# Performance work log

Hardware: AMD Instinct MI355X
Metric: run time of the kernel (lower is better)

Reference implementation:

```python
import jax, jax.numpy as jnp
import numpy as np


def setup_inputs() -> dict:
    key = jax.random.key(0)
    ks = jax.random.split(key, 6)
    B, C, W, H = 8, 512, 64, 64
    return {
        "x": jax.random.normal(ks[0], (B, C, W, H), dtype=jnp.float32),
        "proj_query": jax.random.normal(ks[1], (C, W, H), dtype=jnp.float32),
        "key_w": jax.random.normal(ks[2], (C, C), dtype=jnp.float32) * 0.02,
        "key_b": jax.random.normal(ks[3], (C,), dtype=jnp.float32) * 0.02,
        "value_w": jax.random.normal(ks[4], (C, C), dtype=jnp.float32) * 0.02,
        "value_b": jax.random.normal(ks[5], (C,), dtype=jnp.float32) * 0.02,
        "gamma": jnp.ones((1,), dtype=jnp.float32),
    }


def reference(x, proj_query, key_w, key_b, value_w, value_b, gamma):
    B, C, W, H = x.shape
    N = W * H
    # fixed memory query: (C, N); torch builds B x N x C via permute
    q = proj_query.reshape(C, N)
    # 1x1 convs == per-pixel channel matmuls
    k = jnp.einsum('oc,bchw->bohw', key_w, x) + key_b[None, :, None, None]
    v = jnp.einsum('oc,bchw->bohw', value_w, x) + value_b[None, :, None, None]
    k = k.reshape(B, C, N)
    v = v.reshape(B, C, N)
    # energy = bmm(key [B,C,N], query^T [N,C]) -> B x C x C (channel attention)
    energy = jnp.einsum('bcn,dn->bcd', k, q)
    attention = jax.nn.softmax(energy, axis=-1)
    # out = bmm(attention^T [B,C,C], value [B,C,N]) -> B x C x N
    out = jnp.einsum('bdc,bdn->bcn', attention, v)
    out = out.reshape(B, C, W, H)
    return gamma * out + x
```

## Files before the change

### kernel.cpp

```cpp
#include <hip/hip_runtime.h>

typedef unsigned short u16;
typedef unsigned int u32;
typedef unsigned long long u64;
typedef _Float16 f16x8 __attribute__((ext_vector_type(8)));
typedef float f32x4 __attribute__((ext_vector_type(4)));

__device__ __forceinline__ u16 f2h(float f) {
  union { _Float16 h; u16 u; } c; c.h = (_Float16)f; return c.u;
}
__device__ __forceinline__ float h2f(u16 v) {
  union { u16 u; _Float16 h; } c; c.u = v; return (float)c.h;
}

__device__ __forceinline__ f32x4 mfma16(f16x8 a, f16x8 b, f32x4 c) {
  return __builtin_amdgcn_mfma_f32_16x16x32_f16(a, b, c, 0, 0, 0);
}

__device__ __forceinline__ void ld8f(const float* s, u16* o) {
  float4 a = *(const float4*)s;
  float4 b = *(const float4*)(s + 4);
  o[0] = f2h(a.x); o[1] = f2h(a.y); o[2] = f2h(a.z); o[3] = f2h(a.w);
  o[4] = f2h(b.x); o[5] = f2h(b.y); o[6] = f2h(b.z); o[7] = f2h(b.w);
}

__device__ __forceinline__ void glds16(const u16* g, u16* l) {
  __builtin_amdgcn_global_load_lds(
      reinterpret_cast<const __attribute__((address_space(1))) u32*>(reinterpret_cast<u64>(g)),
      reinterpret_cast<__attribute__((address_space(3))) u32*>(reinterpret_cast<u64>(l)),
      16, 0, 0);
}

template<int TM, int TN, int WM, int WN, int DEPTH>
__device__ __forceinline__ void gemm_core(const u16* __restrict__ A, int lda,
                                          const u16* __restrict__ B, int ldb,
                                          int ksteps, u16* sA, u16* sB, f32x4 acc[TM][TN]) {
  constexpr int NT = WM * WN * 64;
  constexpr int BM = WM * TM * 16, BN = WN * TN * 16;
  constexpr int TILEA = BM * 32, TILEB = BN * 32;
  constexpr int APF = (BM * 4) / NT, BPF = (BN * 4) / NT;
  constexpr int VPI = APF + BPF;
  constexpr int PF = DEPTH - 2;
  static_assert(PF == 1 || PF == 2, "");
  static_assert(APF >= 1 && BPF >= 1, "");

  const int t = threadIdx.x;
  const int lane = t & 63, wave = t >> 6;
  const int wm = wave / WN, wn = wave % WN;
  const int m16 = lane & 15, q4 = lane >> 4;

  int aoff[APF], asl[APF];
#pragma unroll
  for (int p = 0; p < APF; ++p) {
    int s = p * NT + t, row = s >> 2;
    int kc = (s & 3) ^ ((row >> 1) & 3);
    aoff[p] = row * lda + kc * 8;
    asl[p] = (p * NT + (wave << 6)) * 8;
  }
  int boff[BPF], bsl[BPF];
#pragma unroll
  for (int p = 0; p < BPF; ++p) {
    int s = p * NT + t, row = s >> 2;
    int kc = (s & 3) ^ ((row >> 1) & 3);
    boff[p] = row * ldb + kc * 8;
    bsl[p] = (p * NT + (wave << 6)) * 8;
  }

  int aro[TM], bro[TN];
#pragma unroll
  for (int i = 0; i < TM; ++i) {
    int row = wm * TM * 16 + i * 16 + m16;
    aro[i] = row * 32 + ((q4 ^ ((row >> 1) & 3)) << 3);
  }
#pragma unroll
  for (int j = 0; j < TN; ++j) {
    int row = wn * TN * 16 + j * 16 + m16;
    bro[j] = row * 32 + ((q4 ^ ((row >> 1) & 3)) << 3);
  }

#pragma unroll
  for (int j = 0; j < PF; ++j) {
    const u16* Aj = A + j * 32;
    u16* aS = sA + j * TILEA;
#pragma unroll
    for (int p = 0; p < APF; ++p) glds16(Aj + aoff[p], aS + asl[p]);
    const u16* Bj = B + j * 32;
    u16* bS = sB + j * TILEB;
#pragma unroll
    for (int p = 0; p < BPF; ++p) glds16(Bj + boff[p], bS + bsl[p]);
  }

  int cur = 0, stg = PF;
#pragma unroll 1
  for (int kt = 0; kt < ksteps; ++kt) {
    if (kt + PF < ksteps) {
      const u16* An = A + (size_t)(kt + PF) * 32;
      u16* aS = sA + stg * TILEA;
#pragma unroll
      for (int p = 0; p < APF; ++p) glds16(An + aoff[p], aS + asl[p]);
      const u16* Bn = B + (size_t)(kt + PF) * 32;
      u16* bS = sB + stg * TILEB;
#pragma unroll
      for (int p = 0; p < BPF; ++p) glds16(Bn + boff[p], bS + bsl[p]);
    }
    if (PF == 2 && kt + 2 < ksteps)
      asm volatile("s_waitcnt vmcnt(%0)" :: "n"(2 * VPI) : "memory");
    else if (kt + 1 < ksteps)
      asm volatile("s_waitcnt vmcnt(%0)" :: "n"(VPI) : "memory");
    else
      asm volatile("s_waitcnt vmcnt(0)" ::: "memory");
    __builtin_amdgcn_s_barrier();
    __builtin_amdgcn_sched_barrier(0);

    const u16* aR = sA + cur * TILEA;
    const u16* bR = sB + cur * TILEB;
    f16x8 af[TM], bv[TN];
#pragma unroll
    for (int i = 0; i < TM; ++i) af[i] = *(const f16x8*)&aR[aro[i]];
#pragma unroll
    for (int j = 0; j < TN; ++j) bv[j] = *(const f16x8*)&bR[bro[j]];
#pragma unroll
    for (int i = 0; i < TM; ++i)
#pragma unroll
      for (int j = 0; j < TN; ++j)
        acc[i][j] = mfma16(af[i], bv[j], acc[i][j]);

    cur = (cur + 1 == DEPTH) ? 0 : cur + 1;
    stg = (stg + 1 == DEPTH) ? 0 : stg + 1;
  }
}

__global__ __launch_bounds__(256) void prep_all_kernel(const float* __restrict__ x,
                                                       u16* __restrict__ xh, u16* __restrict__ xhT,
                                                       const float* __restrict__ q, u16* __restrict__ qh,
                                                       float* __restrict__ qs,
                                                       const float* __restrict__ vw, u16* __restrict__ vwT,
                                                       const float* __restrict__ kw, u16* __restrict__ kwh,
                                                       float* __restrict__ beta) {
  __shared__ __align__(16) u16 T[64 * 72];
  int blk = blockIdx.x, t = threadIdx.x;
  if (blk < 4096) {
    int nt = blk & 63, ot = (blk >> 6) & 7, b = blk >> 9;
    int s = t & 31;
    int c = (t >> 5) * 8;

    const float* xp = x + ((size_t)b * 512 + ot * 64 + 2 * s) * 4096 + nt * 64 + c;
    u16 r0[8], r1[8];
    ld8f(xp, r0);
    ld8f(xp + 4096, r1);

    u16* xq = xh + ((size_t)b * 512 + ot * 64 + 2 * s) * 4096 + nt * 64 + c;
    *(int4*)xq = *(int4*)r0;
    *(int4*)(xq + 4096) = *(int4*)r1;

    u32* Tw = (u32*)T;
#pragma unroll
    for (int e = 0; e < 8; ++e)
      Tw[(c + e) * 36 + s] = (u32)r0[e] | ((u32)r1[e] << 16);
    __syncthreads();

    int rr = t >> 2, og = t & 3;
    int4 v0 = *(const int4*)&T[rr * 72 + og * 16];
    int4 v1 = *(const int4*)&T[rr * 72 + og * 16 + 8];
    u16* xo = xhT + ((size_t)b * 4096 + nt * 64 + rr) * 512 + ot * 64 + og * 16;
    *(int4*)xo = v0;
    *(int4*)(xo + 8) = v1;
  } else if (blk < 4608) {
    int row = blk - 4096;
    float s = 0.f;
#pragma unroll
    for (int p = 0; p < 2; ++p) {
      size_t i = (size_t)row * 4096 + p * 2048 + t * 8;
      u16 o[8];
      ld8f(q + i, o);
#pragma unroll
      for (int e = 0; e < 8; ++e) s += h2f(o[e]);
      *(int4*)&qh[i] = *(int4*)o;
    }
    for (int off = 32; off; off >>= 1) s += __shfl_xor(s, off);
    __shared__ float wsum[4];
    if ((t & 63) == 0) wsum[t >> 6] = s;
    __syncthreads();
    if (t == 0) qs[row] = wsum[0] + wsum[1] + wsum[2] + wsum[3];
  } else if (blk < 4864) {
    int bi = blk - 4608;
    u16* sT = T;
    int bx = bi & 15, by = bi >> 4;
#pragma unroll
    for (int p = 0; p < 4; ++p) {
      int idx = p * 256 + t; int r = idx >> 5, c = idx & 31;
      sT[r * 33 + c] = f2h(vw[(size_t)(by * 32 + r) * 512 + bx * 32 + c]);
    }
    __syncthreads();
#pragma unroll
    for (int p = 0; p < 4; ++p) {
      int idx = p * 256 + t; int r = idx >> 5, c = idx & 31;
      vwT[(size_t)(bx * 32 + r) * 512 + by * 32 + c] = sT[c * 33 + r];
    }
  } else if (blk < 4992) {
    size_t i = ((size_t)(blk - 4864) * 256 + t) * 8;
    u16 o[8];
    ld8f(kw + i, o);
    *(int4*)&kwh[i] = *(int4*)o;
  } else {
    for (int i = t; i < 4096; i += 256) beta[i] = 0.f;
  }
}

__global__ __launch_bounds__(256) void sgemm_kernel(const u16* __restrict__ qh, const u16* __restrict__ xh,
                                                    u16* __restrict__ Sh) {
  __shared__ __align__(16) u16 sA[4 * 64 * 32], sB[4 * 64 * 32];
  int rt = blockIdx.x, jt = blockIdx.y;
  f32x4 acc[2][2];
#pragma unroll
  for (int i = 0; i < 2; ++i)
#pragma unroll
    for (int j = 0; j < 2; ++j) acc[i][j] = (f32x4){0.f, 0.f, 0.f, 0.f};
  gemm_core<2, 2, 2, 2, 4>(qh + (size_t)jt * 64 * 4096, 4096,
                           xh + (size_t)rt * 64 * 4096, 4096, 128, sA, sB, acc);

  const int t = threadIdx.x, lane = t & 63, wave = t >> 6;
  const int wm = wave >> 1, wn = wave & 1, m16 = lane & 15, q4 = lane >> 4;
  int b = (rt * 64) >> 9, o0 = (rt * 64) & 511;
  u16* Ob = Sh + (size_t)b * 262144;
#pragma unroll
  for (int i = 0; i < 2; ++i)
#pragma unroll
    for (int j = 0; j < 2; ++j)
#pragma unroll
      for (int r = 0; r < 4; ++r) {
        int y = jt * 64 + wm * 32 + i * 16 + q4 * 4 + r;
        int o = o0 + wn * 32 + j * 16 + m16;
        Ob[(size_t)y * 512 + o] = f2h(acc[i][j][r]);
      }
}

__global__ __launch_bounds__(256) void egemm_kernel(const u16* __restrict__ kwh, const u16* __restrict__ Sh,
                                                    float* __restrict__ E) {
  __shared__ __align__(16) u16 sA[4 * 64 * 32], sB[4 * 64 * 32];
  int xt = blockIdx.x >> 3, yt = blockIdx.x & 7, b = blockIdx.y;
  f32x4 acc[2][2];
#pragma unroll
  for (int i = 0; i < 2; ++i)
#pragma unroll
    for (int j = 0; j < 2; ++j) acc[i][j] = (f32x4){0.f, 0.f, 0.f, 0.f};
  gemm_core<2, 2, 2, 2, 4>(kwh + (size_t)xt * 64 * 512, 512,
                           Sh + (size_t)b * 262144 + (size_t)yt * 64 * 512, 512, 16, sA, sB, acc);

  const int t = threadIdx.x, lane = t & 63, wave = t >> 6;
  const int wm = wave >> 1, wn = wave & 1, m16 = lane & 15, q4 = lane >> 4;
  float* O = E + ((size_t)b * 512 + xt * 64) * 512 + yt * 64;
#pragma unroll
  for (int i = 0; i < 2; ++i)
#pragma unroll
    for (int j = 0; j < 2; ++j)
#pragma unroll
      for (int r = 0; r < 4; ++r) {
        int row = wm * 32 + i * 16 + q4 * 4 + r;
        int col = wn * 32 + j * 16 + m16;
        O[(size_t)row * 512 + col] = acc[i][j][r];
      }
}

__global__ __launch_bounds__(256) void softmax_kernel(const float* __restrict__ E, const float* __restrict__ qs,
                                                      const float* __restrict__ kb, const float* __restrict__ vb,
                                                      u16* __restrict__ attT, float* __restrict__ beta) {
  __shared__ float sE[16 * 516];
  __shared__ float sM[16], sS[16];
  int i0 = blockIdx.x * 16, b = blockIdx.y, t = threadIdx.x;
  const float* Eb = E + ((size_t)b * 512 + i0) * 512;
  for (int ch = 0; ch < 32; ++ch) {
    int idx = ch * 256 + t;
    int row = idx >> 9, col = idx & 511;
    sE[row * 516 + col] = Eb[(size_t)row * 512 + col] + kb[i0 + row] * qs[col];
  }
  __syncthreads();
  {
    int row = t >> 4, sub = t & 15;
    float mx = -1e30f;
    for (int ii = 0; ii < 32; ++ii) mx = fmaxf(mx, sE[row * 516 + sub + ii * 16]);
    for (int off = 8; off; off >>= 1) mx = fmaxf(mx, __shfl_xor(mx, off));
    float sm = 0.f;
    for (int ii = 0; ii < 32; ++ii) sm += __expf(sE[row * 516 + sub + ii * 16] - mx);
    for (int off = 8; off; off >>= 1) sm += __shfl_xor(sm, off);
    if (sub == 0) { sM[row] = mx; sS[row] = 1.f / sm; }
  }
  __syncthreads();
  float vbr = vb[i0 + (t & 15)];
  u16* Ob = attT + (size_t)b * 262144;
  for (int ch = 0; ch < 32; ++ch) {
    int idx = ch * 256 + t;
    int r = idx & 15, j = idx >> 4;
    float a = __expf(sE[r * 516 + j] - sM[r]) * sS[r];
    Ob[(size_t)j * 512 + i0 + r] = f2h(a);
    float part = a * vbr;
    for (int off = 8; off; off >>= 1) part += __shfl_xor(part, off);
    if (r == 0) atomicAdd(&beta[b * 512 + j], part);
  }
}

__global__ __launch_bounds__(256) void wgemm_kernel(const u16* __restrict__ attT, const u16* __restrict__ vwT,
                                                    u16* __restrict__ W) {
  __shared__ __align__(16) u16 sA[4 * 64 * 32], sB[4 * 64 * 32];
  int ct = blockIdx.x >> 3, ot = blockIdx.x & 7, b = blockIdx.y;
  f32x4 acc[2][2];
#pragma unroll
  for (int i = 0; i < 2; ++i)
#pragma unroll
    for (int j = 0; j < 2; ++j) acc[i][j] = (f32x4){0.f, 0.f, 0.f, 0.f};
  gemm_core<2, 2, 2, 2, 4>(attT + (size_t)b * 262144 + (size_t)ct * 64 * 512, 512,
                           vwT + (size_t)ot * 64 * 512, 512, 16, sA, sB, acc);

  const int t = threadIdx.x, lane = t & 63, wave = t >> 6;
  const int wm = wave >> 1, wn = wave & 1, m16 = lane & 15, q4 = lane >> 4;
  u16* O = W + (size_t)b * 262144 + (size_t)(ct * 64) * 512 + ot * 64;
#pragma unroll
  for (int i = 0; i < 2; ++i)
#pragma unroll
    for (int j = 0; j < 2; ++j)
#pragma unroll
      for (int r = 0; r < 4; ++r) {
        int row = wm * 32 + i * 16 + q4 * 4 + r;
        int col = wn * 32 + j * 16 + m16;
        O[(size_t)row * 512 + col] = f2h(acc[i][j][r]);
      }
}

__global__ __launch_bounds__(512, 4) void outgemm_kernel(const u16* __restrict__ W, const u16* __restrict__ xhT,
                                                         const float* __restrict__ x, const float* __restrict__ beta,
                                                         const float* __restrict__ gm, float* __restrict__ out) {
  __shared__ __align__(16) u16 sA[3 * 128 * 32], sB[3 * 256 * 32];
  int nt = blockIdx.x, ct = blockIdx.y, b = blockIdx.z;
  f32x4 acc[4][4];
#pragma unroll
  for (int i = 0; i < 4; ++i)
#pragma unroll
    for (int j = 0; j < 4; ++j) acc[i][j] = (f32x4){0.f, 0.f, 0.f, 0.f};
  gemm_core<4, 4, 2, 4, 3>(W + (size_t)b * 262144 + (size_t)ct * 128 * 512, 512,
                           xhT + (size_t)b * 2097152 + (size_t)nt * 256 * 512, 512, 16, sA, sB, acc);

  const int t = threadIdx.x, lane = t & 63, wave = t >> 6;
  const int wm = wave >> 2, wn = wave & 3, m16 = lane & 15, q4 = lane >> 4;
  float g = gm[0];
#pragma unroll
  for (int i = 0; i < 4; ++i)
#pragma unroll
    for (int j = 0; j < 4; ++j)
#pragma unroll
      for (int r = 0; r < 4; ++r) {
        int c = ct * 128 + wm * 64 + i * 16 + q4 * 4 + r;
        int n = nt * 256 + wn * 64 + j * 16 + m16;
        size_t idx = (size_t)b * 2097152 + (size_t)c * 4096 + n;
        out[idx] = g * (acc[i][j][r] + beta[b * 512 + c]) + x[idx];
      }
}

extern "C" void kernel_launch(void* const* d_in, const int* in_sizes, int n_in,
                              void* d_out, int out_size, void* d_ws, size_t ws_size,
                              hipStream_t stream) {
  const float* x  = (const float*)d_in[0];
  const float* pq = (const float*)d_in[1];
  const float* kw = (const float*)d_in[2];
  const float* kb = (const float*)d_in[3];
  const float* vw = (const float*)d_in[4];
  const float* vb = (const float*)d_in[5];
  const float* gm = (const float*)d_in[6];
  float* out = (float*)d_out;

  char* ws = (char*)d_ws;
  u16*   xh   = (u16*)(ws);
  u16*   qh   = (u16*)(ws + (32ull << 20));
  u16*   Sh   = (u16*)(ws + (36ull << 20));
  u16*   W    = (u16*)(ws + (36ull << 20));
  float* E    = (float*)(ws + (40ull << 20));
  u16*   attT = (u16*)(ws + (48ull << 20));
  u16*   kwh  = (u16*)(ws + (52ull << 20));
  u16*   vwT  = (u16*)(ws + (52ull << 20) + 524288);
  char*  sm   = ws + (53ull << 20);
  float* qs   = (float*)(sm);
  float* beta = (float*)(sm + 4096);
  u16*   xhT  = (u16*)(ws + (54ull << 20));

  prep_all_kernel<<<dim3(4993), 256, 0, stream>>>(x, xh, xhT, pq, qh, qs, vw, vwT, kw, kwh, beta);
  sgemm_kernel<<<dim3(64, 8), 256, 0, stream>>>(qh, xh, Sh);
  egemm_kernel<<<dim3(64, 8), 256, 0, stream>>>(kwh, Sh, E);
  softmax_kernel<<<dim3(32, 8), 256, 0, stream>>>(E, qs, kb, vb, attT, beta);
  wgemm_kernel<<<dim3(64, 8), 256, 0, stream>>>(attT, vwT, W);
  outgemm_kernel<<<dim3(16, 4, 8), 512, 0, stream>>>(W, xhT, x, beta, gm, out);
}
```

Before: 241.4 us.

## Loop x-conversion blocks over channel tiles and retile sgemm and outgemm

The x fp16 conversion/transpose now runs one block per (batch, pixel tile) and loops over the 8 channel tiles. It prefetches the next tile's loads into registers and double-buffers the LDS transpose, which cuts block count from 4096 to 512. sgemm moves from 64x64 to 128x128 tiles with 4x4 MFMA accumulators per wave, and outgemm moves from 512-thread 128x256 tiles to 256-thread 128x128 tiles with a 4-stage pipeline. The aim is to improve load overlap and data reuse, at the cost of fewer blocks (less parallelism) in prep and sgemm.

```diff
diff --git a/kernel.cpp b/kernel.cpp
--- a/kernel.cpp
+++ b/kernel.cpp
@@ -20,6 +20,11 @@
 __device__ __forceinline__ void ld8f(const float* s, u16* o) {
   float4 a = *(const float4*)s;
   float4 b = *(const float4*)(s + 4);
+  o[0] = f2h(a.x); o[1] = f2h(a.y); o[2] = f2h(a.z); o[3] = f2h(a.w);
+  o[4] = f2h(b.x); o[5] = f2h(b.y); o[6] = f2h(b.z); o[7] = f2h(b.w);
+}
+
+__device__ __forceinline__ void cvt8(float4 a, float4 b, u16* o) {
   o[0] = f2h(a.x); o[1] = f2h(a.y); o[2] = f2h(a.z); o[3] = f2h(a.w);
   o[4] = f2h(b.x); o[5] = f2h(b.y); o[6] = f2h(b.z); o[7] = f2h(b.w);
 }
@@ -137,36 +142,55 @@
                                                        const float* __restrict__ vw, u16* __restrict__ vwT,
                                                        const float* __restrict__ kw, u16* __restrict__ kwh,
                                                        float* __restrict__ beta) {
-  __shared__ __align__(16) u16 T[64 * 72];
+  __shared__ __align__(16) u16 T[2 * 64 * 72];
   int blk = blockIdx.x, t = threadIdx.x;
-  if (blk < 4096) {
-    int nt = blk & 63, ot = (blk >> 6) & 7, b = blk >> 9;
+  if (blk < 512) {
+    int nt = blk & 63, b = blk >> 6;
     int s = t & 31;
     int c = (t >> 5) * 8;
-
-    const float* xp = x + ((size_t)b * 512 + ot * 64 + 2 * s) * 4096 + nt * 64 + c;
-    u16 r0[8], r1[8];
-    ld8f(xp, r0);
-    ld8f(xp + 4096, r1);
-
-    u16* xq = xh + ((size_t)b * 512 + ot * 64 + 2 * s) * 4096 + nt * 64 + c;
-    *(int4*)xq = *(int4*)r0;
-    *(int4*)(xq + 4096) = *(int4*)r1;
-
-    u32* Tw = (u32*)T;
-#pragma unroll
-    for (int e = 0; e < 8; ++e)
-      Tw[(c + e) * 36 + s] = (u32)r0[e] | ((u32)r1[e] << 16);
-    __syncthreads();
-
+    const float* xbase = x + ((size_t)b * 512 + 2 * s) * 4096 + nt * 64 + c;
     int rr = t >> 2, og = t & 3;
-    int4 v0 = *(const int4*)&T[rr * 72 + og * 16];
-    int4 v1 = *(const int4*)&T[rr * 72 + og * 16 + 8];
-    u16* xo = xhT + ((size_t)b * 4096 + nt * 64 + rr) * 512 + ot * 64 + og * 16;
-    *(int4*)xo = v0;
-    *(int4*)(xo + 8) = v1;
-  } else if (blk < 4608) {
-    int row = blk - 4096;
+
+    float4 ca0 = *(const float4*)xbase;
+    float4 ca1 = *(const float4*)(xbase + 4);
+    float4 cb0 = *(const float4*)(xbase + 4096);
+    float4 cb1 = *(const float4*)(xbase + 4100);
+
+#pragma unroll 1
+    for (int ot = 0; ot < 8; ++ot) {
+      float4 na0, na1, nb0, nb1;
+      if (ot < 7) {
+        const float* np = xbase + (size_t)(ot + 1) * 64 * 4096;
+        na0 = *(const float4*)np;
+        na1 = *(const float4*)(np + 4);
+        nb0 = *(const float4*)(np + 4096);
+        nb1 = *(const float4*)(np + 4100);
+      }
+      u16 r0[8], r1[8];
+      cvt8(ca0, ca1, r0);
+      cvt8(cb0, cb1, r1);
+
+      u16* xq = xh + ((size_t)b * 512 + ot * 64 + 2 * s) * 4096 + nt * 64 + c;
+      *(int4*)xq = *(int4*)r0;
+      *(int4*)(xq + 4096) = *(int4*)r1;
+
+      u32* Tw = (u32*)(T + (ot & 1) * 4608);
+#pragma unroll
+      for (int e = 0; e < 8; ++e)
+        Tw[(c + e) * 36 + s] = (u32)r0[e] | ((u32)r1[e] << 16);
+      __syncthreads();
+
+      const u16* Tr = T + (ot & 1) * 4608;
+      int4 v0 = *(const int4*)&Tr[rr * 72 + og * 16];
+      int4 v1 = *(const int4*)&Tr[rr * 72 + og * 16 + 8];
+      u16* xo = xhT + ((size_t)b * 4096 + nt * 64 + rr) * 512 + ot * 64 + og * 16;
+      *(int4*)xo = v0;
+      *(int4*)(xo + 8) = v1;
+
+      ca0 = na0; ca1 = na1; cb0 = nb0; cb1 = nb1;
+    }
+  } else if (blk < 1024) {
+    int row = blk - 512;
     float s = 0.f;
 #pragma unroll
     for (int p = 0; p < 2; ++p) {
@@ -182,8 +206,8 @@
     if ((t & 63) == 0) wsum[t >> 6] = s;
     __syncthreads();
     if (t == 0) qs[row] = wsum[0] + wsum[1] + wsum[2] + wsum[3];
-  } else if (blk < 4864) {
-    int bi = blk - 4608;
+  } else if (blk < 1280) {
+    int bi = blk - 1024;
     u16* sT = T;
     int bx = bi & 15, by = bi >> 4;
 #pragma unroll
@@ -197,8 +221,8 @@
       int idx = p * 256 + t; int r = idx >> 5, c = idx & 31;
       vwT[(size_t)(bx * 32 + r) * 512 + by * 32 + c] = sT[c * 33 + r];
     }
-  } else if (blk < 4992) {
-    size_t i = ((size_t)(blk - 4864) * 256 + t) * 8;
+  } else if (blk < 1408) {
+    size_t i = ((size_t)(blk - 1280) * 256 + t) * 8;
     u16 o[8];
     ld8f(kw + i, o);
     *(int4*)&kwh[i] = *(int4*)o;
@@ -209,28 +233,28 @@
 
 __global__ __launch_bounds__(256) void sgemm_kernel(const u16* __restrict__ qh, const u16* __restrict__ xh,
                                                     u16* __restrict__ Sh) {
-  __shared__ __align__(16) u16 sA[4 * 64 * 32], sB[4 * 64 * 32];
+  __shared__ __align__(16) u16 sA[4 * 128 * 32], sB[4 * 128 * 32];
   int rt = blockIdx.x, jt = blockIdx.y;
-  f32x4 acc[2][2];
-#pragma unroll
-  for (int i = 0; i < 2; ++i)
-#pragma unroll
-    for (int j = 0; j < 2; ++j) acc[i][j] = (f32x4){0.f, 0.f, 0.f, 0.f};
-  gemm_core<2, 2, 2, 2, 4>(qh + (size_t)jt * 64 * 4096, 4096,
-                           xh + (size_t)rt * 64 * 4096, 4096, 128, sA, sB, acc);
+  f32x4 acc[4][4];
+#pragma unroll
+  for (int i = 0; i < 4; ++i)
+#pragma unroll
+    for (int j = 0; j < 4; ++j) acc[i][j] = (f32x4){0.f, 0.f, 0.f, 0.f};
+  gemm_core<4, 4, 2, 2, 4>(qh + (size_t)jt * 128 * 4096, 4096,
+                           xh + (size_t)rt * 128 * 4096, 4096, 128, sA, sB, acc);
 
   const int t = threadIdx.x, lane = t & 63, wave = t >> 6;
   const int wm = wave >> 1, wn = wave & 1, m16 = lane & 15, q4 = lane >> 4;
-  int b = (rt * 64) >> 9, o0 = (rt * 64) & 511;
+  int b = rt >> 2, o0 = (rt & 3) * 128;
   u16* Ob = Sh + (size_t)b * 262144;
 #pragma unroll
-  for (int i = 0; i < 2; ++i)
-#pragma unroll
-    for (int j = 0; j < 2; ++j)
+  for (int i = 0; i < 4; ++i)
+#pragma unroll
+    for (int j = 0; j < 4; ++j)
 #pragma unroll
       for (int r = 0; r < 4; ++r) {
-        int y = jt * 64 + wm * 32 + i * 16 + q4 * 4 + r;
-        int o = o0 + wn * 32 + j * 16 + m16;
+        int y = jt * 128 + wm * 64 + i * 16 + q4 * 4 + r;
+        int o = o0 + wn * 64 + j * 16 + m16;
         Ob[(size_t)y * 512 + o] = f2h(acc[i][j][r]);
       }
 }
@@ -326,21 +350,21 @@
       }
 }
 
-__global__ __launch_bounds__(512, 4) void outgemm_kernel(const u16* __restrict__ W, const u16* __restrict__ xhT,
-                                                         const float* __restrict__ x, const float* __restrict__ beta,
-                                                         const float* __restrict__ gm, float* __restrict__ out) {
-  __shared__ __align__(16) u16 sA[3 * 128 * 32], sB[3 * 256 * 32];
+__global__ __launch_bounds__(256) void outgemm_kernel(const u16* __restrict__ W, const u16* __restrict__ xhT,
+                                                      const float* __restrict__ x, const float* __restrict__ beta,
+                                                      const float* __restrict__ gm, float* __restrict__ out) {
+  __shared__ __align__(16) u16 sA[4 * 128 * 32], sB[4 * 128 * 32];
   int nt = blockIdx.x, ct = blockIdx.y, b = blockIdx.z;
   f32x4 acc[4][4];
 #pragma unroll
   for (int i = 0; i < 4; ++i)
 #pragma unroll
     for (int j = 0; j < 4; ++j) acc[i][j] = (f32x4){0.f, 0.f, 0.f, 0.f};
-  gemm_core<4, 4, 2, 4, 3>(W + (size_t)b * 262144 + (size_t)ct * 128 * 512, 512,
-                           xhT + (size_t)b * 2097152 + (size_t)nt * 256 * 512, 512, 16, sA, sB, acc);
+  gemm_core<4, 4, 2, 2, 4>(W + (size_t)b * 262144 + (size_t)ct * 128 * 512, 512,
+                           xhT + (size_t)b * 2097152 + (size_t)nt * 128 * 512, 512, 16, sA, sB, acc);
 
   const int t = threadIdx.x, lane = t & 63, wave = t >> 6;
-  const int wm = wave >> 2, wn = wave & 3, m16 = lane & 15, q4 = lane >> 4;
+  const int wm = wave >> 1, wn = wave & 1, m16 = lane & 15, q4 = lane >> 4;
   float g = gm[0];
 #pragma unroll
   for (int i = 0; i < 4; ++i)
@@ -349,7 +373,7 @@
 #pragma unroll
       for (int r = 0; r < 4; ++r) {
         int c = ct * 128 + wm * 64 + i * 16 + q4 * 4 + r;
-        int n = nt * 256 + wn * 64 + j * 16 + m16;
+        int n = nt * 128 + wn * 64 + j * 16 + m16;
         size_t idx = (size_t)b * 2097152 + (size_t)c * 4096 + n;
         out[idx] = g * (acc[i][j][r] + beta[b * 512 + c]) + x[idx];
       }
@@ -381,10 +405,10 @@
   float* beta = (float*)(sm + 4096);
   u16*   xhT  = (u16*)(ws + (54ull << 20));
 
-  prep_all_kernel<<<dim3(4993), 256, 0, stream>>>(x, xh, xhT, pq, qh, qs, vw, vwT, kw, kwh, beta);
-  sgemm_kernel<<<dim3(64, 8), 256, 0, stream>>>(qh, xh, Sh);
+  prep_all_kernel<<<dim3(1409), 256, 0, stream>>>(x, xh, xhT, pq, qh, qs, vw, vwT, kw, kwh, beta);
+  sgemm_kernel<<<dim3(32, 4), 256, 0, stream>>>(qh, xh, Sh);
   egemm_kernel<<<dim3(64, 8), 256, 0, stream>>>(kwh, Sh, E);
   softmax_kernel<<<dim3(32, 8), 256, 0, stream>>>(E, qs, kb, vb, attT, beta);
   wgemm_kernel<<<dim3(64, 8), 256, 0, stream>>>(attT, vwT, W);
-  outgemm_kernel<<<dim3(16, 4, 8), 512, 0, stream>>>(W, xhT, x, beta, gm, out);
-}
+  outgemm_kernel<<<dim3(32, 4, 8), 256, 0, stream>>>(W, xhT, x, beta, gm, out);
+}
```

Measured after the change: 248.5 us. +2.9%, slower.
